# Kernel tuning notes

Measured on AMD Instinct MI355X. Metric: run time of the kernel, lower is better.

The kernel has to match this reference:

```python
import jax, jax.numpy as jnp
import numpy as np

N, E, D, G = 50000, 600000, 128, 1024
NEG_SLOPE = 0.2  # PyG GATConv default negative_slope


def setup_inputs() -> dict:
    key = jax.random.key(0)
    ks = jax.random.split(key, 20)
    s = 1.0 / np.sqrt(D)
    inp = {
        "x": jax.random.normal(ks[0], (N, D), jnp.float32),
        "edge_index": jax.random.randint(ks[1], (2, E), 0, N, dtype=jnp.int64),
        "edge_attr": jax.random.normal(ks[2], (E, 1), jnp.float32),  # ignored (edge_dim=None)
        "batch": jnp.sort(jax.random.randint(ks[3], (N,), 0, G, dtype=jnp.int64)),
    }
    k = 4
    for name in ("g1", "g2", "g3"):
        inp[f"{name}_W"] = jax.random.normal(ks[k], (D, D), jnp.float32) * s; k += 1
        inp[f"{name}_a_src"] = jax.random.normal(ks[k], (D,), jnp.float32) * s; k += 1
        inp[f"{name}_a_dst"] = jax.random.normal(ks[k], (D,), jnp.float32) * s; k += 1
        inp[f"{name}_b"] = jnp.zeros((D,), jnp.float32)
    inp["lin_W"] = jax.random.normal(ks[k], (D, D), jnp.float32) * s
    inp["lin_b"] = jnp.zeros((D,), jnp.float32)
    return inp


def _gat(x, src, dst, W, a_src, a_dst, b):
    # PyG GATConv, heads=1: project, edge attention logits, scatter-softmax over
    # destination nodes, weighted scatter-add aggregation, plus bias.
    n = x.shape[0]
    h = x @ W                                            # [N, D]
    logits = jax.nn.leaky_relu((h @ a_src)[src] + (h @ a_dst)[dst], NEG_SLOPE)  # [E']
    m = jax.ops.segment_max(logits, dst, num_segments=n)
    p = jnp.exp(logits - m[dst])
    denom = jax.ops.segment_sum(p, dst, num_segments=n)
    alpha = p / (denom[dst] + 1e-16)                     # PyG softmax eps
    out = jax.ops.segment_sum(alpha[:, None] * h[src], dst, num_segments=n)
    return out + b


def reference(x, edge_index, edge_attr, batch,
              g1_W, g1_a_src, g1_a_dst, g1_b,
              g2_W, g2_a_src, g2_a_dst, g2_b,
              g3_W, g3_a_src, g3_a_dst, g3_b,
              lin_W, lin_b):
    n = x.shape[0]
    # GATConv default add_self_loops=True
    loop = jnp.arange(n, dtype=edge_index.dtype)
    src = jnp.concatenate([edge_index[0], loop])
    dst = jnp.concatenate([edge_index[1], loop])

    h = jax.nn.relu(_gat(x, src, dst, g1_W, g1_a_src, g1_a_dst, g1_b))
    h = jax.nn.relu(_gat(h, src, dst, g2_W, g2_a_src, g2_a_dst, g2_b))
    h = _gat(h, src, dst, g3_W, g3_a_src, g3_a_dst, g3_b)

    # global_mean_pool over graph ids
    sums = jax.ops.segment_sum(h, batch, num_segments=G)
    cnts = jax.ops.segment_sum(jnp.ones((n,), h.dtype), batch, num_segments=G)
    pooled = sums / jnp.maximum(cnts, 1.0)[:, None]
    # dropout(p=0.5) is identity in eval mode
    return pooled @ lin_W + lin_b
```

## Files before the change

### kernel.cpp

```cpp
#include <hip/hip_runtime.h>

#define D 128
typedef unsigned short ushort_t;
typedef __attribute__((ext_vector_type(8))) short bf16x8;
typedef __attribute__((ext_vector_type(4))) float f32x4;

__device__ __forceinline__ float wred_max(float v){
#pragma unroll
  for (int o = 1; o < 64; o <<= 1) v = fmaxf(v, __shfl_xor(v, o, 64));
  return v;
}
__device__ __forceinline__ float wred_sum(float v){
#pragma unroll
  for (int o = 1; o < 64; o <<= 1) v += __shfl_xor(v, o, 64);
  return v;
}
__device__ __forceinline__ unsigned short f2bf(float f){
  unsigned u = __float_as_uint(f);
  unsigned r = (u + 0x7FFFu + ((u >> 16) & 1u)) >> 16;
  return (unsigned short)r;
}
__device__ __forceinline__ float bflo(unsigned u){ return __uint_as_float(u << 16); }
__device__ __forceinline__ float bfhi(unsigned u){ return __uint_as_float(u & 0xFFFF0000u); }

__global__ __launch_bounds__(256) void k_init(const float* __restrict__ W0,
                                              const float* __restrict__ W1,
                                              const float* __restrict__ W2,
                                              ushort_t* __restrict__ Wp,
                                              int* __restrict__ cnt, int n){
  int b = blockIdx.x;
  if (b < 192){
    int wi = b >> 6;
    const float* W = wi == 0 ? W0 : (wi == 1 ? W1 : W2);
    ushort_t* dst = Wp + wi * 32768;
    int idx = (b & 63) * 256 + threadIdx.x;
    int k = idx >> 7, c = idx & 127;
    float w = W[idx];
    unsigned short hi = f2bf(w);
    float r = w - __uint_as_float((unsigned)hi << 16);
    int ct = c >> 4, s = k >> 5, lane = (c & 15) | (((k >> 3) & 3) << 4), e = k & 7;
    int off = ((ct * 4 + s) * 64 + lane) * 8 + e;
    dst[off] = hi;
    dst[16384 + off] = f2bf(r);
  } else {
    int i = (b - 192) * 256 + threadIdx.x;
    if (i < n) cnt[i] = 0;
  }
}

template<bool XF32>
__device__ __forceinline__ void gemm_body(int bid, const void* __restrict__ Av,
                                          const ushort_t* __restrict__ Wp,
                                          const float* __restrict__ a_src,
                                          const float* __restrict__ a_dst,
                                          ushort_t* __restrict__ Hbf,
                                          float* __restrict__ as_,
                                          float* __restrict__ ad_,
                                          int n){
  int tid = threadIdx.x;
  int wid = tid >> 6, l = tid & 63;
  int kg = l >> 4, cin = l & 15;
  int r0 = bid * 64 + wid * 16;
  int row_l = r0 + cin;
  if (row_l > n - 1) row_l = n - 1;

  bf16x8 ah[4];
  if (XF32){
    const float* xp = (const float*)Av + (size_t)row_l * D + kg * 8;
#pragma unroll
    for (int s = 0; s < 4; s++){
      float4 f0 = *(const float4*)(xp + s * 32);
      float4 f1 = *(const float4*)(xp + s * 32 + 4);
      ah[s][0] = (short)f2bf(f0.x); ah[s][1] = (short)f2bf(f0.y);
      ah[s][2] = (short)f2bf(f0.z); ah[s][3] = (short)f2bf(f0.w);
      ah[s][4] = (short)f2bf(f1.x); ah[s][5] = (short)f2bf(f1.y);
      ah[s][6] = (short)f2bf(f1.z); ah[s][7] = (short)f2bf(f1.w);
    }
  } else {
    const ushort_t* xp = (const ushort_t*)Av + (size_t)row_l * D + kg * 8;
#pragma unroll
    for (int s = 0; s < 4; s++) ah[s] = *(const bf16x8*)(xp + s * 32);
  }

  const bf16x8* Bh = (const bf16x8*)Wp;
  const bf16x8* Bl = (const bf16x8*)(Wp + 16384);

  f32x4 acc[8];
#pragma unroll
  for (int ct = 0; ct < 8; ct++) acc[ct] = (f32x4){0.f, 0.f, 0.f, 0.f};

#pragma unroll
  for (int ct = 0; ct < 8; ct++)
#pragma unroll
    for (int s = 0; s < 4; s++){
      acc[ct] = __builtin_amdgcn_mfma_f32_16x16x32_bf16(ah[s], Bh[(ct * 4 + s) * 64 + l], acc[ct], 0, 0, 0);
      acc[ct] = __builtin_amdgcn_mfma_f32_16x16x32_bf16(ah[s], Bl[(ct * 4 + s) * 64 + l], acc[ct], 0, 0, 0);
    }

  float asv[8], adv[8];
#pragma unroll
  for (int ct = 0; ct < 8; ct++){
    asv[ct] = a_src[ct * 16 + cin];
    adv[ct] = a_dst[ct * 16 + cin];
  }
#pragma unroll
  for (int j = 0; j < 4; j++){
    float ps = 0.f, pd = 0.f;
#pragma unroll
    for (int ct = 0; ct < 8; ct++){ ps += acc[ct][j] * asv[ct]; pd += acc[ct][j] * adv[ct]; }
#pragma unroll
    for (int o = 1; o < 16; o <<= 1){ ps += __shfl_xor(ps, o, 64); pd += __shfl_xor(pd, o, 64); }
    int row = r0 + kg * 4 + j;
    if (row < n){
      if (cin == 0) as_[row] = ps;
      if (cin == 1) ad_[row] = pd;
#pragma unroll
      for (int ct = 0; ct < 8; ct++)
        Hbf[(size_t)row * D + ct * 16 + cin] = f2bf(acc[ct][j]);
    }
  }
}

__global__ __launch_bounds__(256) void k_gemm_mfma_bf(const void* __restrict__ Av,
                                                      const ushort_t* __restrict__ Wp,
                                                      const float* __restrict__ a_src,
                                                      const float* __restrict__ a_dst,
                                                      ushort_t* __restrict__ Hbf,
                                                      float* __restrict__ as_,
                                                      float* __restrict__ ad_,
                                                      int n){
  gemm_body<false>(blockIdx.x, Av, Wp, a_src, a_dst, Hbf, as_, ad_, n);
}

__global__ __launch_bounds__(256) void k_gemm1_fill(const float* __restrict__ x,
                                                    const ushort_t* __restrict__ Wp,
                                                    const float* __restrict__ a_src,
                                                    const float* __restrict__ a_dst,
                                                    ushort_t* __restrict__ Hbf,
                                                    float* __restrict__ as_,
                                                    float* __restrict__ ad_,
                                                    int n, int gemm_grid,
                                                    const int* __restrict__ src,
                                                    const int* __restrict__ dst,
                                                    int E,
                                                    int* __restrict__ cnt,
                                                    ushort_t* __restrict__ csr_pad){
  int b = blockIdx.x;
  if (b < gemm_grid){
    gemm_body<true>(b, x, Wp, a_src, a_dst, Hbf, as_, ad_, n);
  } else {
    int e = (b - gemm_grid) * 256 + threadIdx.x;
    if (e >= E) return;
    int s = src[e], d = dst[e];
    int slot = atomicAdd(&cnt[d], 1);
    if (slot < 63) csr_pad[((size_t)d << 6) + slot] = (ushort_t)s;
  }
}

template<bool OUTBF>
__global__ __launch_bounds__(256) void k_agg(const uint4* __restrict__ hb4,
                                             const ushort_t* __restrict__ csr_pad,
                                             const int* __restrict__ cnt,
                                             const float* __restrict__ asrc,
                                             const float* __restrict__ adst,
                                             const float* __restrict__ bias,
                                             ushort_t* __restrict__ outb,
                                             float* __restrict__ outf,
                                             int relu, int n){
  int node = (blockIdx.x * 256 + threadIdx.x) >> 6;
  if (node >= n) return;
  int lane = threadIdx.x & 63;
  int q = lane & 15, g = lane >> 4;
  int degr = cnt[node]; if (degr > 63) degr = 63;
  int degp = degr + 1;
  const ushort_t* eb = csr_pad + ((size_t)node << 6);
  float adn = adst[node];

  int s = node; float logit = -1e30f;
  if (lane < degr) s = eb[lane];
  if (lane <= degr){
    float xx = asrc[s] + adn;
    logit = xx >= 0.f ? xx : 0.2f * xx;
  }
  float m = wred_max(logit);
  float p = (lane <= degr) ? __expf(logit - m) : 0.f;
  float denom = wred_sum(p);
  float inv = 1.f / (denom + 1e-16f);

  float acc[8] = {0.f, 0.f, 0.f, 0.f, 0.f, 0.f, 0.f, 0.f};
#pragma unroll 2
  for (int j = 0; j < degp; j += 4){
    int slot = j + g;
    int   sj = __shfl(s, slot, 64);
    float wj = (slot < degp) ? __shfl(p, slot, 64) : 0.f;
    uint4 v = hb4[(size_t)sj * 16 + q];
    acc[0] += wj * bflo(v.x); acc[1] += wj * bfhi(v.x);
    acc[2] += wj * bflo(v.y); acc[3] += wj * bfhi(v.y);
    acc[4] += wj * bflo(v.z); acc[5] += wj * bfhi(v.z);
    acc[6] += wj * bflo(v.w); acc[7] += wj * bfhi(v.w);
  }

#pragma unroll
  for (int o = 16; o < 64; o <<= 1){
#pragma unroll
    for (int i = 0; i < 8; i++) acc[i] += __shfl_xor(acc[i], o, 64);
  }

  if (g == 0){
    float4 b0 = *(const float4*)&bias[q * 8];
    float4 b1 = *(const float4*)&bias[q * 8 + 4];
    float o0 = acc[0] * inv + b0.x, o1 = acc[1] * inv + b0.y;
    float o2 = acc[2] * inv + b0.z, o3 = acc[3] * inv + b0.w;
    float o4 = acc[4] * inv + b1.x, o5 = acc[5] * inv + b1.y;
    float o6 = acc[6] * inv + b1.z, o7 = acc[7] * inv + b1.w;
    if (relu){
      o0 = fmaxf(o0, 0.f); o1 = fmaxf(o1, 0.f); o2 = fmaxf(o2, 0.f); o3 = fmaxf(o3, 0.f);
      o4 = fmaxf(o4, 0.f); o5 = fmaxf(o5, 0.f); o6 = fmaxf(o6, 0.f); o7 = fmaxf(o7, 0.f);
    }
    if (OUTBF){
      ushort4 u0, u1;
      u0.x = f2bf(o0); u0.y = f2bf(o1); u0.z = f2bf(o2); u0.w = f2bf(o3);
      u1.x = f2bf(o4); u1.y = f2bf(o5); u1.z = f2bf(o6); u1.w = f2bf(o7);
      *(ushort4*)&outb[(size_t)node * D + q * 8]     = u0;
      *(ushort4*)&outb[(size_t)node * D + q * 8 + 4] = u1;
    } else {
      *(float4*)&outf[(size_t)node * D + q * 8]     = make_float4(o0, o1, o2, o3);
      *(float4*)&outf[(size_t)node * D + q * 8 + 4] = make_float4(o4, o5, o6, o7);
    }
  }
}

__device__ __forceinline__ int lbound(const int* a, int n, int key){
  int lo = 0, hi = n;
  while (lo < hi){ int mid = (lo + hi) >> 1; if (a[mid] < key) lo = mid + 1; else hi = mid; }
  return lo;
}

__global__ __launch_bounds__(128) void k_pool_final(const float* __restrict__ x,
                                                    const int* __restrict__ batch,
                                                    const float* __restrict__ Wl,
                                                    const float* __restrict__ bl,
                                                    float* __restrict__ out, int n){
  __shared__ float pl[128];
  int g = blockIdx.x;
  int c = threadIdx.x;
  int lo = lbound(batch, n, g);
  int hi = lbound(batch, n, g + 1);
  float sum = 0.f;
  for (int i = lo; i < hi; i++) sum += x[(size_t)i * D + c];
  float cnt = (float)(hi - lo);
  pl[c] = sum / fmaxf(cnt, 1.f);
  __syncthreads();
  float acc = bl[c];
#pragma unroll 4
  for (int k = 0; k < 128; k++) acc += pl[k] * Wl[(size_t)k * D + c];
  out[(size_t)g * D + c] = acc;
}

extern "C" void kernel_launch(void* const* d_in, const int* in_sizes, int n_in,
                              void* d_out, int out_size, void* d_ws, size_t ws_size,
                              hipStream_t stream){
  const float* x     = (const float*)d_in[0];
  const int*   ei    = (const int*)d_in[1];
  const int*   batch = (const int*)d_in[3];
  const float* gW[3]  = {(const float*)d_in[4],  (const float*)d_in[8],  (const float*)d_in[12]};
  const float* gAs[3] = {(const float*)d_in[5],  (const float*)d_in[9],  (const float*)d_in[13]};
  const float* gAd[3] = {(const float*)d_in[6],  (const float*)d_in[10], (const float*)d_in[14]};
  const float* gB[3]  = {(const float*)d_in[7],  (const float*)d_in[11], (const float*)d_in[15]};
  const float* linW = (const float*)d_in[16];
  const float* linB = (const float*)d_in[17];
  float* outp = (float*)d_out;

  int N  = in_sizes[3];
  int E  = in_sizes[1] / 2;
  int G  = out_size / D;

  char* ws = (char*)d_ws;
  size_t off = 0;
  auto alloc = [&](size_t bytes)->void*{
    void* p = ws + off;
    off += (bytes + 255) & ~(size_t)255;
    return p;
  };
  float*    bufF    = (float*)alloc((size_t)N * D * 4);
  ushort_t* bufB    = (ushort_t*)alloc((size_t)N * D * 2);
  ushort_t* Hbf     = (ushort_t*)alloc((size_t)N * D * 2);
  float*    as_     = (float*)alloc((size_t)N * 4);
  float*    ad_     = (float*)alloc((size_t)N * 4);
  int*      cnt     = (int*)  alloc((size_t)N * 4);
  ushort_t* csr_pad = (ushort_t*)alloc((size_t)N * 64 * 2);
  ushort_t* Wp      = (ushort_t*)alloc(3 * 2 * 16384 * 2);
  (void)ws_size; (void)n_in;

  const int* esrc = ei;
  const int* edst = ei + E;

  int tpb = 256;
  int egrid = (E + tpb - 1) / tpb;
  int ngrid = (N + tpb - 1) / tpb;
  int gemm_grid = (N + 63) / 64;
  int node_grid = (N + 3) / 4;

  k_init<<<192 + ngrid, tpb, 0, stream>>>(gW[0], gW[1], gW[2], Wp, cnt, N);

  const uint4* hbu = (const uint4*)Hbf;

  k_gemm1_fill<<<gemm_grid + egrid, tpb, 0, stream>>>(x, Wp, gAs[0], gAd[0], Hbf, as_, ad_, N,
                                                      gemm_grid, esrc, edst, E, cnt, csr_pad);
  k_agg<true>  <<<node_grid, tpb, 0, stream>>>(hbu, csr_pad, cnt, as_, ad_, gB[0], bufB, nullptr, 1, N);
  k_gemm_mfma_bf<<<gemm_grid, tpb, 0, stream>>>(bufB, Wp + 32768, gAs[1], gAd[1], Hbf, as_, ad_, N);
  k_agg<true>  <<<node_grid, tpb, 0, stream>>>(hbu, csr_pad, cnt, as_, ad_, gB[1], bufB, nullptr, 1, N);
  k_gemm_mfma_bf<<<gemm_grid, tpb, 0, stream>>>(bufB, Wp + 65536, gAs[2], gAd[2], Hbf, as_, ad_, N);
  k_agg<false> <<<node_grid, tpb, 0, stream>>>(hbu, csr_pad, cnt, as_, ad_, gB[2], nullptr, bufF, 0, N);

  k_pool_final<<<G, 128, 0, stream>>>(bufF, batch, linW, linB, outp, N);
}
```

Before: 227.3 us.

## Split activations instead of weights in bf16 GEMM and slice CSR fill by destination

Weights are now stored only as single bf16 (no hi/lo split). The first-layer GEMM splits the fp32 input into hi/lo bf16 parts, so it still runs two MFMAs per step, while layers 2 and 3 drop to one MFMA and skip the low weight load. Weight precision falls from an effective ~16 mantissa bits to bf16, which may affect accuracy. The edge-bucketing fill now has each block scan 2048 edges and handle only the destinations in one of 8 node slices, which localises atomics and csr writes. The cost is reading every dst index eight times.

Result: faster. 211.1 us (-7.2%).

```diff
diff --git a/kernel.cpp b/kernel.cpp
--- a/kernel.cpp
+++ b/kernel.cpp
@@ -32,16 +32,11 @@
   if (b < 192){
     int wi = b >> 6;
     const float* W = wi == 0 ? W0 : (wi == 1 ? W1 : W2);
-    ushort_t* dst = Wp + wi * 32768;
+    ushort_t* dst = Wp + wi * 16384;
     int idx = (b & 63) * 256 + threadIdx.x;
     int k = idx >> 7, c = idx & 127;
-    float w = W[idx];
-    unsigned short hi = f2bf(w);
-    float r = w - __uint_as_float((unsigned)hi << 16);
     int ct = c >> 4, s = k >> 5, lane = (c & 15) | (((k >> 3) & 3) << 4), e = k & 7;
-    int off = ((ct * 4 + s) * 64 + lane) * 8 + e;
-    dst[off] = hi;
-    dst[16384 + off] = f2bf(r);
+    dst[((ct * 4 + s) * 64 + lane) * 8 + e] = f2bf(W[idx]);
   } else {
     int i = (b - 192) * 256 + threadIdx.x;
     if (i < n) cnt[i] = 0;
@@ -64,17 +59,21 @@
   int row_l = r0 + cin;
   if (row_l > n - 1) row_l = n - 1;
 
-  bf16x8 ah[4];
+  bf16x8 ah[4], al[4];
   if (XF32){
     const float* xp = (const float*)Av + (size_t)row_l * D + kg * 8;
 #pragma unroll
     for (int s = 0; s < 4; s++){
       float4 f0 = *(const float4*)(xp + s * 32);
       float4 f1 = *(const float4*)(xp + s * 32 + 4);
-      ah[s][0] = (short)f2bf(f0.x); ah[s][1] = (short)f2bf(f0.y);
-      ah[s][2] = (short)f2bf(f0.z); ah[s][3] = (short)f2bf(f0.w);
-      ah[s][4] = (short)f2bf(f1.x); ah[s][5] = (short)f2bf(f1.y);
-      ah[s][6] = (short)f2bf(f1.z); ah[s][7] = (short)f2bf(f1.w);
+      float fv[8] = {f0.x, f0.y, f0.z, f0.w, f1.x, f1.y, f1.z, f1.w};
+#pragma unroll
+      for (int e = 0; e < 8; e++){
+        unsigned short h = f2bf(fv[e]);
+        ah[s][e] = (short)h;
+        float r = fv[e] - __uint_as_float((unsigned)h << 16);
+        al[s][e] = (short)f2bf(r);
+      }
     }
   } else {
     const ushort_t* xp = (const ushort_t*)Av + (size_t)row_l * D + kg * 8;
@@ -83,7 +82,6 @@
   }
 
   const bf16x8* Bh = (const bf16x8*)Wp;
-  const bf16x8* Bl = (const bf16x8*)(Wp + 16384);
 
   f32x4 acc[8];
 #pragma unroll
@@ -93,8 +91,10 @@
   for (int ct = 0; ct < 8; ct++)
 #pragma unroll
     for (int s = 0; s < 4; s++){
-      acc[ct] = __builtin_amdgcn_mfma_f32_16x16x32_bf16(ah[s], Bh[(ct * 4 + s) * 64 + l], acc[ct], 0, 0, 0);
-      acc[ct] = __builtin_amdgcn_mfma_f32_16x16x32_bf16(ah[s], Bl[(ct * 4 + s) * 64 + l], acc[ct], 0, 0, 0);
+      bf16x8 bh = Bh[(ct * 4 + s) * 64 + l];
+      acc[ct] = __builtin_amdgcn_mfma_f32_16x16x32_bf16(ah[s], bh, acc[ct], 0, 0, 0);
+      if (XF32)
+        acc[ct] = __builtin_amdgcn_mfma_f32_16x16x32_bf16(al[s], bh, acc[ct], 0, 0, 0);
     }
 
   float asv[8], adv[8];
@@ -142,18 +142,31 @@
                                                     int n, int gemm_grid,
                                                     const int* __restrict__ src,
                                                     const int* __restrict__ dst,
-                                                    int E,
+                                                    int E, int sliceN,
                                                     int* __restrict__ cnt,
                                                     ushort_t* __restrict__ csr_pad){
   int b = blockIdx.x;
   if (b < gemm_grid){
     gemm_body<true>(b, x, Wp, a_src, a_dst, Hbf, as_, ad_, n);
   } else {
-    int e = (b - gemm_grid) * 256 + threadIdx.x;
-    if (e >= E) return;
-    int s = src[e], d = dst[e];
-    int slot = atomicAdd(&cnt[d], 1);
-    if (slot < 63) csr_pad[((size_t)d << 6) + slot] = (ushort_t)s;
+    int f = b - gemm_grid;
+    int chunk = f >> 3;
+    int slice = b & 7;
+    int d_lo = slice * sliceN;
+    int d_hi = d_lo + sliceN;
+    int e0 = chunk * 2048 + (int)threadIdx.x;
+#pragma unroll
+    for (int i = 0; i < 8; i++){
+      int e = e0 + i * 256;
+      if (e < E){
+        int d = dst[e];
+        if (d >= d_lo && d < d_hi){
+          int s = src[e];
+          int slot = atomicAdd(&cnt[d], 1);
+          if (slot < 63) csr_pad[((size_t)d << 6) + slot] = (ushort_t)s;
+        }
+      }
+    }
   }
 }
 
@@ -199,7 +212,6 @@
     acc[4] += wj * bflo(v.z); acc[5] += wj * bfhi(v.z);
     acc[6] += wj * bflo(v.w); acc[7] += wj * bfhi(v.w);
   }
-
 #pragma unroll
   for (int o = 16; o < 64; o <<= 1){
 #pragma unroll
@@ -289,28 +301,29 @@
   float*    ad_     = (float*)alloc((size_t)N * 4);
   int*      cnt     = (int*)  alloc((size_t)N * 4);
   ushort_t* csr_pad = (ushort_t*)alloc((size_t)N * 64 * 2);
-  ushort_t* Wp      = (ushort_t*)alloc(3 * 2 * 16384 * 2);
+  ushort_t* Wp      = (ushort_t*)alloc(3 * 16384 * 2);
   (void)ws_size; (void)n_in;
 
   const int* esrc = ei;
   const int* edst = ei + E;
 
   int tpb = 256;
-  int egrid = (E + tpb - 1) / tpb;
   int ngrid = (N + tpb - 1) / tpb;
   int gemm_grid = (N + 63) / 64;
   int node_grid = (N + 3) / 4;
+  int nchunk = (E + 2047) / 2048;
+  int sliceN = (N + 7) / 8;
 
   k_init<<<192 + ngrid, tpb, 0, stream>>>(gW[0], gW[1], gW[2], Wp, cnt, N);
 
   const uint4* hbu = (const uint4*)Hbf;
 
-  k_gemm1_fill<<<gemm_grid + egrid, tpb, 0, stream>>>(x, Wp, gAs[0], gAd[0], Hbf, as_, ad_, N,
-                                                      gemm_grid, esrc, edst, E, cnt, csr_pad);
+  k_gemm1_fill<<<gemm_grid + nchunk * 8, tpb, 0, stream>>>(x, Wp, gAs[0], gAd[0], Hbf, as_, ad_, N,
+                                                           gemm_grid, esrc, edst, E, sliceN, cnt, csr_pad);
   k_agg<true>  <<<node_grid, tpb, 0, stream>>>(hbu, csr_pad, cnt, as_, ad_, gB[0], bufB, nullptr, 1, N);
-  k_gemm_mfma_bf<<<gemm_grid, tpb, 0, stream>>>(bufB, Wp + 32768, gAs[1], gAd[1], Hbf, as_, ad_, N);
+  k_gemm_mfma_bf<<<gemm_grid, tpb, 0, stream>>>(bufB, Wp + 16384, gAs[1], gAd[1], Hbf, as_, ad_, N);
   k_agg<true>  <<<node_grid, tpb, 0, stream>>>(hbu, csr_pad, cnt, as_, ad_, gB[1], bufB, nullptr, 1, N);
-  k_gemm_mfma_bf<<<gemm_grid, tpb, 0, stream>>>(bufB, Wp + 65536, gAs[2], gAd[2], Hbf, as_, ad_, N);
+  k_gemm_mfma_bf<<<gemm_grid, tpb, 0, stream>>>(bufB, Wp + 32768, gAs[2], gAd[2], Hbf, as_, ad_, N);
   k_agg<false> <<<node_grid, tpb, 0, stream>>>(hbu, csr_pad, cnt, as_, ad_, gB[2], nullptr, bufF, 0, N);
 
   k_pool_final<<<G, 128, 0, stream>>>(bufF, batch, linW, linB, outp, N);
```
